# Optimization experiments

Measured on AMD Instinct MI355X. Metric: run time of the kernel, lower is better.

The kernel has to match this reference:

```python
import jax, jax.numpy as jnp
import numpy as np

D_MODEL = 768
NUM_HEADS = 12
HEAD_DIM = D_MODEL // NUM_HEADS
BATCH = 1
SEQ = 4096


def setup_inputs() -> dict:
    key = jax.random.key(0)
    ks = jax.random.split(key, 11)
    s = 0.02
    return {
        "q": jax.random.normal(ks[0], (BATCH, SEQ, D_MODEL), jnp.float32),
        "k": jax.random.normal(ks[1], (BATCH, SEQ, D_MODEL), jnp.float32),
        "v": jax.random.normal(ks[2], (BATCH, SEQ, D_MODEL), jnp.float32),
        "Wq": jax.random.normal(ks[3], (D_MODEL, D_MODEL), jnp.float32) * s,
        "bq": jnp.zeros((D_MODEL,), jnp.float32),
        "Wk": jax.random.normal(ks[4], (D_MODEL, D_MODEL), jnp.float32) * s,
        "bk": jnp.zeros((D_MODEL,), jnp.float32),
        "Wv": jax.random.normal(ks[5], (D_MODEL, D_MODEL), jnp.float32) * s,
        "bv": jnp.zeros((D_MODEL,), jnp.float32),
        "Wo": jax.random.normal(ks[6], (D_MODEL, D_MODEL), jnp.float32) * s,
        "bo": jnp.zeros((D_MODEL,), jnp.float32),
    }


def reference(q, k, v, Wq, bq, Wk, bk, Wv, bv, Wo, bo):
    B, S, D = q.shape
    H, Hd = NUM_HEADS, HEAD_DIM
    # linear projections (torch Linear: x @ W.T + b)
    qh = (q @ Wq.T + bq).reshape(B, S, H, Hd).transpose(0, 2, 1, 3)  # [B,H,S,Hd]
    kh = (k @ Wk.T + bk).reshape(B, S, H, Hd).transpose(0, 2, 1, 3)
    vh = (v @ Wv.T + bv).reshape(B, S, H, Hd).transpose(0, 2, 1, 3)
    scale = 1.0 / jnp.sqrt(jnp.asarray(Hd, qh.dtype))
    scores = jnp.einsum("bhsd,bhtd->bhst", qh, kh) * scale  # [B,H,S,S]
    weights = jax.nn.softmax(scores, axis=-1)
    attn = jnp.einsum("bhst,bhtd->bhsd", weights, vh)  # [B,H,S,Hd]
    attn = attn.transpose(0, 2, 1, 3).reshape(B, S, D)
    return attn @ Wo.T + bo
```

## Files before the change

kernel.cpp:

```cpp
#include <hip/hip_runtime.h>

#define S_LEN 4096
#define DMODEL 768
#define NHEAD 12
#define HD 64

typedef __bf16 bf16x8 __attribute__((ext_vector_type(8)));
typedef __bf16 bf16x4 __attribute__((ext_vector_type(4)));
typedef float f32x4 __attribute__((ext_vector_type(4)));
typedef float f32x16 __attribute__((ext_vector_type(16)));
typedef unsigned short u16x8 __attribute__((ext_vector_type(8)));
typedef unsigned short u16x4 __attribute__((ext_vector_type(4)));
typedef _Float16 f16x4 __attribute__((ext_vector_type(4)));

#if __has_builtin(__builtin_amdgcn_exp2f)
#define EXP2F(x) __builtin_amdgcn_exp2f(x)
#else
#define EXP2F(x) exp2f(x)
#endif

#define MFMA32(a, b, c) __builtin_amdgcn_mfma_f32_32x32x16_bf16(a, b, c, 0, 0, 0)

__device__ __forceinline__ unsigned short f2bf(float f) {
  unsigned int u = __float_as_uint(f);
  u += 0x7fffu + ((u >> 16) & 1u);
  return (unsigned short)(u >> 16);
}

__device__ __forceinline__ void gload_lds16(const void* g, void* l) {
  __builtin_amdgcn_global_load_lds(
      (__attribute__((address_space(1))) void*)g,
      (__attribute__((address_space(3))) void*)l, 16, 0, 0);
}

struct CvtArgs {
  const float* src[4];
  unsigned short* dst[4];
};

__global__ __launch_bounds__(256) void cvt_kernel(CvtArgs a) {
  const int seg = blockIdx.y;
  const int i = (blockIdx.x * 256 + threadIdx.x) * 8;
  const float* s = a.src[seg] + i;
  u16x8 o;
#pragma unroll
  for (int j = 0; j < 8; ++j) o[j] = f2bf(s[j]);
  *reinterpret_cast<u16x8*>(a.dst[seg] + i) = o;
}

struct QkvArgs {
  const float* A[3];
  const unsigned short* W[3];
  const float* bias[3];
  unsigned short* dst[3];
  float scale[3];
};

__global__ __launch_bounds__(256) void qkv_gemm(QkvArgs a) {
  __shared__ unsigned char lds[32768];
  const int z = blockIdx.z;
  const float* __restrict__ A = a.A[z];
  const unsigned short* __restrict__ B = a.W[z];
  const float* __restrict__ bias = a.bias[z];
  unsigned short* __restrict__ dst = a.dst[z];
  const float scale = a.scale[z];

  const int tid = threadIdx.x;
  const int lane = tid & 63;
  const int w = tid >> 6;
  const int wr = w >> 1, wc = w & 1;
  const int c = lane & 15, g = lane >> 4;
  const int m0 = blockIdx.x * 128;
  const int n0 = blockIdx.y * 128;

  f32x4 acc[4][4] = {};

  for (int kt = 0; kt < DMODEL / 64; ++kt) {
#pragma unroll
    for (int p = 0; p < 4; ++p) {
      const int te = p * 256 + tid;
      const int row = te >> 3;
      const int sb = ((te & 7) * 16) ^ ((row & 7) << 4);
      const float* src = A + (size_t)(m0 + row) * DMODEL + kt * 64 + (sb >> 1);
      const f32x4 lo = *reinterpret_cast<const f32x4*>(src);
      const f32x4 hi = *reinterpret_cast<const f32x4*>(src + 4);
      bf16x8 v;
#pragma unroll
      for (int j = 0; j < 4; ++j) { v[j] = (__bf16)lo[j]; v[4 + j] = (__bf16)hi[j]; }
      *reinterpret_cast<bf16x8*>(&lds[te * 16]) = v;
    }
#pragma unroll
    for (int p = 0; p < 4; ++p) {
      const int te = p * 256 + tid;
      const int row = te >> 3;
      const int sb = ((te & 7) * 16) ^ ((row & 7) << 4);
      gload_lds16(B + (size_t)(n0 + row) * DMODEL + kt * 64 + (sb >> 1),
                  &lds[16384 + te * 16]);
    }
    __syncthreads();

    bf16x8 af[4][2], bfr[4][2];
#pragma unroll
    for (int mb = 0; mb < 4; ++mb)
#pragma unroll
      for (int ks = 0; ks < 2; ++ks) {
        const int row = wr * 64 + mb * 16 + c;
        const int byte = (ks * 64 + g * 16) ^ ((row & 7) << 4);
        af[mb][ks] = *reinterpret_cast<const bf16x8*>(&lds[row * 128 + byte]);
      }
#pragma unroll
    for (int nb = 0; nb < 4; ++nb)
#pragma unroll
      for (int ks = 0; ks < 2; ++ks) {
        const int row = wc * 64 + nb * 16 + c;
        const int byte = (ks * 64 + g * 16) ^ ((row & 7) << 4);
        bfr[nb][ks] = *reinterpret_cast<const bf16x8*>(&lds[16384 + row * 128 + byte]);
      }
    __builtin_amdgcn_s_setprio(1);
#pragma unroll
    for (int ks = 0; ks < 2; ++ks)
#pragma unroll
      for (int mb = 0; mb < 4; ++mb)
#pragma unroll
        for (int nb = 0; nb < 4; ++nb)
          acc[mb][nb] = __builtin_amdgcn_mfma_f32_16x16x32_bf16(
              af[mb][ks], bfr[nb][ks], acc[mb][nb], 0, 0, 0);
    __builtin_amdgcn_s_setprio(0);
    __syncthreads();
  }

#pragma unroll
  for (int mb = 0; mb < 4; ++mb) {
#pragma unroll
    for (int nb = 0; nb < 4; ++nb) {
      const int n = n0 + wc * 64 + nb * 16 + c;
      const float bv = bias[n];
#pragma unroll
      for (int r = 0; r < 4; ++r) {
        const int m = m0 + wr * 64 + mb * 16 + g * 4 + r;
        const float v = (acc[mb][nb][r] + bv) * scale;
        const int hh = n >> 6, hd = n & 63;
        if (z != 2) {
          dst[((size_t)hh * S_LEN + m) * HD + hd] = f2bf(v);
        } else {
          const int mp = (m & ~12) | ((m & 4) << 1) | ((m & 8) >> 1);
          dst[((size_t)hh * HD + hd) * S_LEN + mp] = f2bf(v);
        }
      }
    }
  }
}

__global__ __launch_bounds__(256) void gemm_out(
    const unsigned short* __restrict__ A, const unsigned short* __restrict__ B,
    const float* __restrict__ bias, float* __restrict__ dst) {
  __shared__ unsigned char lds[32768];
  const int tid = threadIdx.x;
  const int lane = tid & 63;
  const int w = tid >> 6;
  const int wr = w >> 1, wc = w & 1;
  const int c = lane & 15, g = lane >> 4;
  const int m0 = blockIdx.x * 128;
  const int n0 = blockIdx.y * 128;

  f32x4 acc[4][4] = {};

  for (int kt = 0; kt < DMODEL / 64; ++kt) {
#pragma unroll
    for (int p = 0; p < 4; ++p) {
      const int te = p * 256 + tid;
      const int row = te >> 3;
      const int sb = ((te & 7) * 16) ^ ((row & 7) << 4);
      gload_lds16(A + (size_t)(m0 + row) * DMODEL + kt * 64 + (sb >> 1), &lds[te * 16]);
      gload_lds16(B + (size_t)(n0 + row) * DMODEL + kt * 64 + (sb >> 1), &lds[16384 + te * 16]);
    }
    __syncthreads();

    bf16x8 af[4][2], bfr[4][2];
#pragma unroll
    for (int mb = 0; mb < 4; ++mb)
#pragma unroll
      for (int ks = 0; ks < 2; ++ks) {
        const int row = wr * 64 + mb * 16 + c;
        const int byte = (ks * 64 + g * 16) ^ ((row & 7) << 4);
        af[mb][ks] = *reinterpret_cast<const bf16x8*>(&lds[row * 128 + byte]);
      }
#pragma unroll
    for (int nb = 0; nb < 4; ++nb)
#pragma unroll
      for (int ks = 0; ks < 2; ++ks) {
        const int row = wc * 64 + nb * 16 + c;
        const int byte = (ks * 64 + g * 16) ^ ((row & 7) << 4);
        bfr[nb][ks] = *reinterpret_cast<const bf16x8*>(&lds[16384 + row * 128 + byte]);
      }
    __builtin_amdgcn_s_setprio(1);
#pragma unroll
    for (int ks = 0; ks < 2; ++ks)
#pragma unroll
      for (int mb = 0; mb < 4; ++mb)
#pragma unroll
        for (int nb = 0; nb < 4; ++nb)
          acc[mb][nb] = __builtin_amdgcn_mfma_f32_16x16x32_bf16(
              af[mb][ks], bfr[nb][ks], acc[mb][nb], 0, 0, 0);
    __builtin_amdgcn_s_setprio(0);
    __syncthreads();
  }

#pragma unroll
  for (int mb = 0; mb < 4; ++mb)
#pragma unroll
    for (int nb = 0; nb < 4; ++nb) {
      const int n = n0 + wc * 64 + nb * 16 + c;
      const float bv = bias[n];
#pragma unroll
      for (int r = 0; r < 4; ++r) {
        const int m = m0 + wr * 64 + mb * 16 + g * 4 + r;
        dst[(size_t)m * DMODEL + n] = acc[mb][nb][r] + bv;
      }
    }
}

__global__ __launch_bounds__(512, 4) void attn_kernel(
    const unsigned short* __restrict__ qh,
    const unsigned short* __restrict__ kh,
    const unsigned short* __restrict__ vtp,
    _Float16* __restrict__ pacc,
    float* __restrict__ prs) {
  __shared__ unsigned char lds[49152];
  const int tid = threadIdx.x;
  const int lane = tid & 63;
  const int w = tid >> 6;
  const int c5 = lane & 31;
  const int h2 = lane >> 5;
  const int hh = blockIdx.y;
  const int split = blockIdx.z;
  const int qw = blockIdx.x * 256 + w * 32;
  const int kv0 = split * (S_LEN / 4);
  const int nkt = (S_LEN / 4) / 64;

  bf16x8 qa[4];
#pragma unroll
  for (int ks = 0; ks < 4; ++ks)
    qa[ks] = *reinterpret_cast<const bf16x8*>(
        qh + ((size_t)hh * S_LEN + qw + c5) * HD + ks * 16 + h2 * 8);

  const unsigned short* ksrc =
      kh + ((size_t)hh * S_LEN + kv0 + (tid & 63)) * HD + (tid >> 6) * 8;
  const unsigned short* vsrc =
      vtp + ((size_t)hh * HD + (tid & 63)) * S_LEN + kv0 + (tid >> 6) * 8;
  const int dL = tid * 16;

  auto stage = [&](int bo) {
    gload_lds16(ksrc, &lds[bo + dL]);
    gload_lds16(vsrc, &lds[bo + 8192 + dL]);
    ksrc += 64 * HD;
    vsrc += 64;
  };

  stage(0);
  stage(16384);

  f32x16 accO[2] = {};
  float rs0 = 0.f, rs1 = 0.f, rs2 = 0.f, rs3 = 0.f;

  auto compute = [&](const unsigned char* Kb, const unsigned char* Vb) {
    f32x16 s0 = {}, s1 = {};
    __builtin_amdgcn_s_setprio(1);
#pragma unroll
    for (int ks = 0; ks < 4; ++ks) {
      const unsigned char* kbase = Kb + (ks * 2 + h2) * 1024 + c5 * 16;
      const bf16x8 k0 = *reinterpret_cast<const bf16x8*>(kbase);
      const bf16x8 k1 = *reinterpret_cast<const bf16x8*>(kbase + 512);
      s0 = MFMA32(k0, qa[ks], s0);
      s1 = MFMA32(k1, qa[ks], s1);
    }
    __builtin_amdgcn_s_setprio(0);

#pragma unroll
    for (int t = 0; t < 2; ++t)
#pragma unroll
      for (int ss = 0; ss < 2; ++ss) {
        const unsigned char* vbase = Vb + (t * 4 + ss * 2 + h2) * 1024 + c5 * 16;
        const bf16x8 va0 = *reinterpret_cast<const bf16x8*>(vbase);
        const bf16x8 va1 = *reinterpret_cast<const bf16x8*>(vbase + 512);
        bf16x8 pb;
        float racc = 0.f;
#pragma unroll
        for (int r = 0; r < 8; ++r) {
          const float e = EXP2F(t ? s1[ss * 8 + r] : s0[ss * 8 + r]);
          racc += e;
          pb[r] = (__bf16)e;
        }
        if (t == 0) { if (ss == 0) rs0 += racc; else rs1 += racc; }
        else        { if (ss == 0) rs2 += racc; else rs3 += racc; }
        __builtin_amdgcn_s_setprio(1);
        accO[0] = MFMA32(va0, pb, accO[0]);
        accO[1] = MFMA32(va1, pb, accO[1]);
        __builtin_amdgcn_s_setprio(0);
      }
  };

  int boC = 0;
  int boS = 32768;
  for (int t = 0; t < nkt; ++t) {
    if (t + 2 < nkt) {
      asm volatile("s_waitcnt vmcnt(2)" ::: "memory");
      __builtin_amdgcn_sched_barrier(0);
      __builtin_amdgcn_s_barrier();
      __builtin_amdgcn_sched_barrier(0);
      stage(boS);
    } else if (t + 1 < nkt) {
      asm volatile("s_waitcnt vmcnt(2)" ::: "memory");
      __builtin_amdgcn_sched_barrier(0);
      __builtin_amdgcn_s_barrier();
      __builtin_amdgcn_sched_barrier(0);
    } else {
      asm volatile("s_waitcnt vmcnt(0)" ::: "memory");
      __builtin_amdgcn_sched_barrier(0);
      __builtin_amdgcn_s_barrier();
      __builtin_amdgcn_sched_barrier(0);
    }
    compute(&lds[boC], &lds[boC + 8192]);
    boC += 16384; if (boC == 49152) boC = 0;
    boS += 16384; if (boS == 49152) boS = 0;
  }

  float rsA = (rs0 + rs1) + (rs2 + rs3);
  rsA += __shfl_xor(rsA, 32);
  const size_t hqbase = ((size_t)split * NHEAD + hh) * S_LEN + qw + c5;
  if (h2 == 0) prs[hqbase] = rsA * 0.015625f;
#pragma unroll
  for (int dt = 0; dt < 2; ++dt)
#pragma unroll
    for (int rr = 0; rr < 4; ++rr) {
      f16x4 o;
#pragma unroll
      for (int j = 0; j < 4; ++j)
        o[j] = (_Float16)(accO[dt][rr * 4 + j] * 0.015625f);
      *reinterpret_cast<f16x4*>(
          pacc + hqbase * 64 + dt * 32 + rr * 8 + h2 * 4) = o;
    }
}

__global__ __launch_bounds__(256) void combine_kernel(
    const _Float16* __restrict__ pacc, const float* __restrict__ prs,
    unsigned short* __restrict__ attb) {
  const int idx = blockIdx.x * 256 + threadIdx.x;
  const int hq = idx >> 4;
  const int d4 = (idx & 15) * 4;
  const int h = hq >> 12;
  const int q = hq & 4095;
  const int HS = NHEAD * S_LEN;
  const size_t o0 = (size_t)hq * 64 + d4;
  float acc4[4] = {0.f, 0.f, 0.f, 0.f};
  float rs = 0.f;
#pragma unroll
  for (int k = 0; k < 4; ++k) {
    const f16x4 av = *reinterpret_cast<const f16x4*>(pacc + o0 + (size_t)k * HS * 64);
#pragma unroll
    for (int j = 0; j < 4; ++j) acc4[j] += (float)av[j];
    rs += prs[hq + k * HS];
  }
  const float inv = 1.f / rs;
  u16x4 ov;
#pragma unroll
  for (int j = 0; j < 4; ++j) ov[j] = f2bf(acc4[j] * inv);
  *reinterpret_cast<u16x4*>(attb + (size_t)q * DMODEL + h * HD + d4) = ov;
}

extern "C" void kernel_launch(void* const* d_in, const int* in_sizes, int n_in,
                              void* d_out, int out_size, void* d_ws, size_t ws_size,
                              hipStream_t stream) {
  (void)in_sizes; (void)n_in; (void)out_size;
  const float* q  = (const float*)d_in[0];
  const float* k  = (const float*)d_in[1];
  const float* v  = (const float*)d_in[2];
  const float* Wq = (const float*)d_in[3];
  const float* bq = (const float*)d_in[4];
  const float* Wk = (const float*)d_in[5];
  const float* bk = (const float*)d_in[6];
  const float* Wv = (const float*)d_in[7];
  const float* bv = (const float*)d_in[8];
  const float* Wo = (const float*)d_in[9];
  const float* bo = (const float*)d_in[10];
  float* out = (float*)d_out;

  const size_t SD = (size_t)S_LEN * DMODEL;
  const size_t DD = (size_t)DMODEL * DMODEL;
  if (ws_size < (7 * SD + 4 * DD) * 2) return;

  unsigned short* ws   = (unsigned short*)d_ws;
  unsigned short* wqb  = ws;
  unsigned short* wkb  = ws + DD;
  unsigned short* wvb  = ws + 2 * DD;
  unsigned short* qhb  = ws + 4 * SD;
  unsigned short* khb  = ws + 5 * SD;
  unsigned short* vtb  = ws + 6 * SD;
  float*          prs  = (float*)(ws + 7 * SD);
  unsigned short* wob  = ws + 7 * SD + 393216;
  _Float16*       pacc = (_Float16*)ws;
  unsigned short* attb = ws + 4 * SD;

  CvtArgs ca;
  ca.src[0] = Wq; ca.dst[0] = wqb;
  ca.src[1] = Wk; ca.dst[1] = wkb;
  ca.src[2] = Wv; ca.dst[2] = wvb;
  ca.src[3] = Wo; ca.dst[3] = wob;
  cvt_kernel<<<dim3(288, 4), 256, 0, stream>>>(ca);

  QkvArgs qa;
  qa.A[0] = q; qa.W[0] = wqb; qa.bias[0] = bq; qa.dst[0] = qhb;
  qa.scale[0] = 0.18033688011112042f;
  qa.A[1] = k; qa.W[1] = wkb; qa.bias[1] = bk; qa.dst[1] = khb;
  qa.scale[1] = 1.0f;
  qa.A[2] = v; qa.W[2] = wvb; qa.bias[2] = bv; qa.dst[2] = vtb;
  qa.scale[2] = 1.0f;
  qkv_gemm<<<dim3(32, 6, 3), 256, 0, stream>>>(qa);

  attn_kernel<<<dim3(S_LEN / 256, NHEAD, 4), 512, 0, stream>>>(
      qhb, khb, vtb, pacc, prs);

  combine_kernel<<<dim3((NHEAD * S_LEN * 16) / 256), 256, 0, stream>>>(
      pacc, prs, attb);

  gemm_out<<<dim3(32, 6), 256, 0, stream>>>(attb, wob, bo, out);
}
```

Before: 121.9 us.

## Have each attention wave process 64 query rows to reuse K/V fragments

Each wave now handles two 32-row query tiles, so the block shrinks from 512 to 256 threads. Every K and V fragment read from LDS feeds two MFMAs instead of one, which halves LDS reads per unit of compute, and staging issues two async loads per thread per buffer. The cost is roughly double the accumulator and score registers per wave, so fewer waves fit per CU to hide latency.

```diff
diff --git a/kernel.cpp b/kernel.cpp
--- a/kernel.cpp
+++ b/kernel.cpp
@@ -6,7 +6,6 @@
 #define HD 64
 
 typedef __bf16 bf16x8 __attribute__((ext_vector_type(8)));
-typedef __bf16 bf16x4 __attribute__((ext_vector_type(4)));
 typedef float f32x4 __attribute__((ext_vector_type(4)));
 typedef float f32x16 __attribute__((ext_vector_type(16)));
 typedef unsigned short u16x8 __attribute__((ext_vector_type(8)));
@@ -220,7 +219,7 @@
     }
 }
 
-__global__ __launch_bounds__(512, 4) void attn_kernel(
+__global__ __launch_bounds__(256, 2) void attn_kernel(
     const unsigned short* __restrict__ qh,
     const unsigned short* __restrict__ kh,
     const unsigned short* __restrict__ vtp,
@@ -234,15 +233,18 @@
   const int h2 = lane >> 5;
   const int hh = blockIdx.y;
   const int split = blockIdx.z;
-  const int qw = blockIdx.x * 256 + w * 32;
+  const int qw = blockIdx.x * 256 + w * 64;
   const int kv0 = split * (S_LEN / 4);
   const int nkt = (S_LEN / 4) / 64;
 
-  bf16x8 qa[4];
-#pragma unroll
-  for (int ks = 0; ks < 4; ++ks)
-    qa[ks] = *reinterpret_cast<const bf16x8*>(
+  bf16x8 qa0[4], qa1[4];
+#pragma unroll
+  for (int ks = 0; ks < 4; ++ks) {
+    qa0[ks] = *reinterpret_cast<const bf16x8*>(
         qh + ((size_t)hh * S_LEN + qw + c5) * HD + ks * 16 + h2 * 8);
+    qa1[ks] = *reinterpret_cast<const bf16x8*>(
+        qh + ((size_t)hh * S_LEN + qw + 32 + c5) * HD + ks * 16 + h2 * 8);
+  }
 
   const unsigned short* ksrc =
       kh + ((size_t)hh * S_LEN + kv0 + (tid & 63)) * HD + (tid >> 6) * 8;
@@ -252,7 +254,9 @@
 
   auto stage = [&](int bo) {
     gload_lds16(ksrc, &lds[bo + dL]);
+    gload_lds16(ksrc + 32, &lds[bo + 4096 + dL]);
     gload_lds16(vsrc, &lds[bo + 8192 + dL]);
+    gload_lds16(vsrc + 32, &lds[bo + 12288 + dL]);
     ksrc += 64 * HD;
     vsrc += 64;
   };
@@ -260,19 +264,21 @@
   stage(0);
   stage(16384);
 
-  f32x16 accO[2] = {};
-  float rs0 = 0.f, rs1 = 0.f, rs2 = 0.f, rs3 = 0.f;
+  f32x16 accO00 = {}, accO01 = {}, accO10 = {}, accO11 = {};
+  float rsA = 0.f, rsB = 0.f;
 
   auto compute = [&](const unsigned char* Kb, const unsigned char* Vb) {
-    f32x16 s0 = {}, s1 = {};
+    f32x16 s0A = {}, s1A = {}, s0B = {}, s1B = {};
     __builtin_amdgcn_s_setprio(1);
 #pragma unroll
     for (int ks = 0; ks < 4; ++ks) {
       const unsigned char* kbase = Kb + (ks * 2 + h2) * 1024 + c5 * 16;
       const bf16x8 k0 = *reinterpret_cast<const bf16x8*>(kbase);
       const bf16x8 k1 = *reinterpret_cast<const bf16x8*>(kbase + 512);
-      s0 = MFMA32(k0, qa[ks], s0);
-      s1 = MFMA32(k1, qa[ks], s1);
+      s0A = MFMA32(k0, qa0[ks], s0A);
+      s0B = MFMA32(k0, qa1[ks], s0B);
+      s1A = MFMA32(k1, qa0[ks], s1A);
+      s1B = MFMA32(k1, qa1[ks], s1B);
     }
     __builtin_amdgcn_s_setprio(0);
 
@@ -283,19 +289,22 @@
         const unsigned char* vbase = Vb + (t * 4 + ss * 2 + h2) * 1024 + c5 * 16;
         const bf16x8 va0 = *reinterpret_cast<const bf16x8*>(vbase);
         const bf16x8 va1 = *reinterpret_cast<const bf16x8*>(vbase + 512);
-        bf16x8 pb;
-        float racc = 0.f;
+        bf16x8 pbA, pbB;
+        float ra = 0.f, rb = 0.f;
 #pragma unroll
         for (int r = 0; r < 8; ++r) {
-          const float e = EXP2F(t ? s1[ss * 8 + r] : s0[ss * 8 + r]);
-          racc += e;
-          pb[r] = (__bf16)e;
+          const float eA = EXP2F(t ? s1A[ss * 8 + r] : s0A[ss * 8 + r]);
+          const float eB = EXP2F(t ? s1B[ss * 8 + r] : s0B[ss * 8 + r]);
+          ra += eA; rb += eB;
+          pbA[r] = (__bf16)eA;
+          pbB[r] = (__bf16)eB;
         }
-        if (t == 0) { if (ss == 0) rs0 += racc; else rs1 += racc; }
-        else        { if (ss == 0) rs2 += racc; else rs3 += racc; }
+        rsA += ra; rsB += rb;
         __builtin_amdgcn_s_setprio(1);
-        accO[0] = MFMA32(va0, pb, accO[0]);
-        accO[1] = MFMA32(va1, pb, accO[1]);
+        accO00 = MFMA32(va0, pbA, accO00);
+        accO01 = MFMA32(va1, pbA, accO01);
+        accO10 = MFMA32(va0, pbB, accO10);
+        accO11 = MFMA32(va1, pbB, accO11);
         __builtin_amdgcn_s_setprio(0);
       }
   };
@@ -304,13 +313,13 @@
   int boS = 32768;
   for (int t = 0; t < nkt; ++t) {
     if (t + 2 < nkt) {
-      asm volatile("s_waitcnt vmcnt(2)" ::: "memory");
+      asm volatile("s_waitcnt vmcnt(4)" ::: "memory");
       __builtin_amdgcn_sched_barrier(0);
       __builtin_amdgcn_s_barrier();
       __builtin_amdgcn_sched_barrier(0);
       stage(boS);
     } else if (t + 1 < nkt) {
-      asm volatile("s_waitcnt vmcnt(2)" ::: "memory");
+      asm volatile("s_waitcnt vmcnt(4)" ::: "memory");
       __builtin_amdgcn_sched_barrier(0);
       __builtin_amdgcn_s_barrier();
       __builtin_amdgcn_sched_barrier(0);
@@ -325,20 +334,27 @@
     boS += 16384; if (boS == 49152) boS = 0;
   }
 
-  float rsA = (rs0 + rs1) + (rs2 + rs3);
   rsA += __shfl_xor(rsA, 32);
-  const size_t hqbase = ((size_t)split * NHEAD + hh) * S_LEN + qw + c5;
-  if (h2 == 0) prs[hqbase] = rsA * 0.015625f;
+  rsB += __shfl_xor(rsB, 32);
+  const size_t hqb0 = ((size_t)split * NHEAD + hh) * S_LEN + qw + c5;
+  const size_t hqb1 = hqb0 + 32;
+  if (h2 == 0) {
+    prs[hqb0] = rsA * 0.015625f;
+    prs[hqb1] = rsB * 0.015625f;
+  }
 #pragma unroll
   for (int dt = 0; dt < 2; ++dt)
 #pragma unroll
     for (int rr = 0; rr < 4; ++rr) {
-      f16x4 o;
-#pragma unroll
-      for (int j = 0; j < 4; ++j)
-        o[j] = (_Float16)(accO[dt][rr * 4 + j] * 0.015625f);
-      *reinterpret_cast<f16x4*>(
-          pacc + hqbase * 64 + dt * 32 + rr * 8 + h2 * 4) = o;
+      const int doff = dt * 32 + rr * 8 + h2 * 4;
+      f16x4 oA, oB;
+#pragma unroll
+      for (int j = 0; j < 4; ++j) {
+        oA[j] = (_Float16)((dt ? accO01[rr * 4 + j] : accO00[rr * 4 + j]) * 0.015625f);
+        oB[j] = (_Float16)((dt ? accO11[rr * 4 + j] : accO10[rr * 4 + j]) * 0.015625f);
+      }
+      *reinterpret_cast<f16x4*>(pacc + hqb0 * 64 + doff) = oA;
+      *reinterpret_cast<f16x4*>(pacc + hqb1 * 64 + doff) = oB;
     }
 }
 
@@ -417,7 +433,7 @@
   qa.scale[2] = 1.0f;
   qkv_gemm<<<dim3(32, 6, 3), 256, 0, stream>>>(qa);
 
-  attn_kernel<<<dim3(S_LEN / 256, NHEAD, 4), 512, 0, stream>>>(
+  attn_kernel<<<dim3(S_LEN / 256, NHEAD, 4), 256, 0, stream>>>(
       qhb, khb, vtb, pacc, prs);
 
   combine_kernel<<<dim3((NHEAD * S_LEN * 16) / 256), 256, 0, stream>>>(
```

Result: no change. 121.4 us (median of 2 runs) (-0.4%).
